# Performance work log

Measured on AMD Instinct MI355X. Metric: run time of the kernel, lower is better.

## Reference

```python
import jax, jax.numpy as jnp
import numpy as np

BS, T, N, M, P = 1024, 128, 128, 256, 256


def _lstm_cell(xin, h, c, Wih, Whh, bih, bhh):
    # PyTorch LSTMCell: gates ordered i, f, g, o
    z = xin @ Wih.T + bih + h @ Whh.T + bhh
    i, f, g, o = jnp.split(z, 4, axis=1)
    i = jax.nn.sigmoid(i); f = jax.nn.sigmoid(f)
    g = jnp.tanh(g); o = jax.nn.sigmoid(o)
    c2 = f * c + i * g
    return o * jnp.tanh(c2), c2


def setup_inputs() -> dict:
    key = jax.random.key(0)
    ks = jax.random.split(key, 24)
    s = 0.05
    return {
        "x": jax.random.normal(ks[0], (BS, T, N), jnp.float32),
        "y_known": jax.random.normal(ks[1], (BS, T, 1), jnp.float32),
        "We": jax.random.normal(ks[2], (T, 2 * M), jnp.float32) * s,
        "Ue": jax.random.normal(ks[3], (T, T), jnp.float32) * s,
        "Ve": jax.random.normal(ks[4], (1, T), jnp.float32) * s,
        "Wih_e": jax.random.normal(ks[5], (4 * M, N), jnp.float32) * s,
        "Whh_e": jax.random.normal(ks[6], (4 * M, M), jnp.float32) * s,
        "bih_e": jax.random.normal(ks[7], (4 * M,), jnp.float32) * s,
        "bhh_e": jax.random.normal(ks[8], (4 * M,), jnp.float32) * s,
        "Wd": jax.random.normal(ks[9], (M, 2 * P), jnp.float32) * s,
        "Ud": jax.random.normal(ks[10], (M, M), jnp.float32) * s,
        "Vd": jax.random.normal(ks[11], (1, M), jnp.float32) * s,
        "Wih_d": jax.random.normal(ks[12], (4 * P, 1), jnp.float32) * s,
        "Whh_d": jax.random.normal(ks[13], (4 * P, P), jnp.float32) * s,
        "bih_d": jax.random.normal(ks[14], (4 * P,), jnp.float32) * s,
        "bhh_d": jax.random.normal(ks[15], (4 * P,), jnp.float32) * s,
        "Wt": jax.random.normal(ks[16], (1, M + 1), jnp.float32) * s,
        "bt": jax.random.normal(ks[17], (1,), jnp.float32) * s,
        "W1": jax.random.normal(ks[18], (P, P + M), jnp.float32) * s,
        "b1": jax.random.normal(ks[19], (P,), jnp.float32) * s,
        "W2": jax.random.normal(ks[20], (1, P), jnp.float32) * s,
        "b2": jax.random.normal(ks[21], (1,), jnp.float32) * s,
    }


def reference(x, y_known, We, Ue, Ve, Wih_e, Whh_e, bih_e, bhh_e,
              Wd, Ud, Vd, Wih_d, Whh_d, bih_d, bhh_d,
              Wt, bt, W1, b1, W2, b2):
    bs, Tl, n = x.shape
    m = Whh_e.shape[1]
    p = Whh_d.shape[1]

    # ---- encoder (input attention) ----
    # U_e(x.permute(0,2,1)): loop-invariant, hoisted. (bs, n, T)
    Ux = jnp.einsum('btn,st->bns', x, Ue)

    def enc_step(carry, _):
        h, s = carry
        hs = jnp.concatenate([h, s], axis=1)            # (bs, 2m)
        ohs = hs @ We.T                                  # (bs, T)
        tanh_sum = jnp.tanh(ohs[:, None, :] + Ux)        # (bs, n, T)
        e = jnp.einsum('bnt,t->bn', tanh_sum, Ve[0])     # (bs, n)
        alpha = jax.nn.softmax(e, axis=1)
        xt = alpha * e                                   # faithful quirk: alpha * e_t
        h2, s2 = _lstm_cell(xt, h, s, Wih_e, Whh_e, bih_e, bhh_e)
        return (h2, s2), h2

    z = jnp.zeros((bs, m), x.dtype)
    _, h_all = jax.lax.scan(enc_step, (z, z), None, length=Tl)
    x1 = jnp.transpose(h_all, (1, 2, 0))                 # (bs, m, T)

    # ---- decoder (temporal attention) ----
    Udx = jnp.einsum('bmt,km->btk', x1, Ud)              # (bs, T, m)

    def dec_step(carry, yt):
        d, s, _ = carry
        ds = jnp.concatenate([d, s], axis=1)             # (bs, 2p)
        ods = ds @ Wd.T                                   # (bs, m)
        tanh_sum = jnp.tanh(ods[:, None, :] + Udx)        # (bs, T, m)
        l = jnp.einsum('btm,m->bt', tanh_sum, Vd[0])      # (bs, T)
        beta = jax.nn.softmax(l, axis=1)
        c = jnp.einsum('bt,bmt->bm', beta, x1)            # (bs, m)
        y_tilde = jnp.concatenate([yt, c], axis=1) @ Wt.T + bt  # (bs, 1)
        d2, s2 = _lstm_cell(y_tilde, d, s, Wih_d, Whh_d, bih_d, bhh_d)
        return (d2, s2, c), None

    zp = jnp.zeros((bs, p), x.dtype)
    zc = jnp.zeros((bs, m), x.dtype)
    (d, _, c), _ = jax.lax.scan(dec_step, (zp, zp, zc),
                                jnp.transpose(y_known, (1, 0, 2)))
    out1 = jnp.concatenate([d, c], axis=1) @ W1.T + b1
    return out1 @ W2.T + b2
```

## Files before the change

kernel.cpp:

```cpp
#include <hip/hip_runtime.h>


typedef unsigned int   uint;
typedef unsigned short ushort;
typedef _Float16 h2v __attribute__((ext_vector_type(2)));

#define O_WEH     0u
#define O_WENCH   32768u
#define O_WDH     229376u
#define O_WHHDH   294912u
#define O_UDT     425984u
#define O_UET     491520u
#define O_W1T     507904u
#define O_BENC    638976u
#define O_BDEC    640000u
#define W_FLOATS  641024u
#define O_X1H     641024u
#define O_BUF     17418240u
#define WS_FLOATS 34195456u

#define C2E 2.8853900817779268f
#define L2E 1.4426950408889634f

#define FMA4(acc, s, w) \
  acc.x = fmaf((s), (w).x, acc.x); \
  acc.y = fmaf((s), (w).y, acc.y); \
  acc.z = fmaf((s), (w).z, acc.z); \
  acc.w = fmaf((s), (w).w, acc.w);

union H2U { uint u; h2v h; _Float16 hs[2]; };

__device__ __forceinline__ float fdot2u(uint w, uint s, float acc) {
  H2U a; a.u = w; H2U b; b.u = s;
  return __builtin_amdgcn_fdot2(a.h, b.h, acc, false);
}
__device__ __forceinline__ uint pk2(float lo, float hi) {
  H2U v; v.hs[0] = (_Float16)lo; v.hs[1] = (_Float16)hi; return v.u;
}
__device__ __forceinline__ float h2lo(uint u) { H2U v; v.u = u; return (float)v.hs[0]; }
__device__ __forceinline__ float h2hi(uint u) { H2U v; v.u = u; return (float)v.hs[1]; }

__device__ __forceinline__ float fsig(float x) {
  return __builtin_amdgcn_rcpf(1.f + __builtin_amdgcn_exp2f(-L2E * x));
}
__device__ __forceinline__ float fth(float x) {
  float r = __builtin_amdgcn_rcpf(1.f + __builtin_amdgcn_exp2f(C2E * x));
  return fmaf(-2.f, r, 1.f);
}

#define DOT8(w, s0, s1) { \
  a0 = fdot2u(w.x, s0, a0); a1 = fdot2u(w.y, s0, a1); \
  a2 = fdot2u(w.z, s0, a2); a3 = fdot2u(w.w, s0, a3); \
  b0 = fdot2u(w.x, s1, b0); b1 = fdot2u(w.y, s1, b1); \
  b2 = fdot2u(w.z, s1, b2); b3 = fdot2u(w.w, s1, b3); }

#define ATT_TERM(vv, uu, oo) \
  ((vv) * __builtin_amdgcn_rcpf(1.f + __builtin_amdgcn_exp2f(fmaf(C2E, (uu), (oo)))))

__global__ __launch_bounds__(256) void prep_k(
    const float* __restrict__ We,    const float* __restrict__ Wih_e,
    const float* __restrict__ Whh_e, const float* __restrict__ Wd,
    const float* __restrict__ Whh_d, const float* __restrict__ W1,
    const float* __restrict__ Ud,    const float* __restrict__ Ue,
    const float* __restrict__ bih_e, const float* __restrict__ bhh_e,
    const float* __restrict__ bih_d, const float* __restrict__ bhh_d,
    float* __restrict__ ws)
{
  uint* wsu = (uint*)ws;
  unsigned idx = blockIdx.x * 256u + threadIdx.x;
  if (idx >= W_FLOATS) return;
  if (idx < 32768u) {
    unsigned kp = idx >> 7, j = idx & 127u;
    wsu[O_WEH + idx] = pk2(We[j * 512u + 2u*kp], We[j * 512u + 2u*kp + 1u]);
  } else if (idx < 229376u) {
    unsigned rel = idx - 32768u;
    unsigned kp = rel >> 10, j = rel & 1023u;
    float v0, v1;
    if (kp < 64u) { v0 = Wih_e[j * 128u + 2u*kp];          v1 = Wih_e[j * 128u + 2u*kp + 1u]; }
    else { unsigned k0 = 2u*(kp - 64u); v0 = Whh_e[j * 256u + k0]; v1 = Whh_e[j * 256u + k0 + 1u]; }
    wsu[O_WENCH + rel] = pk2(v0, v1);
  } else if (idx < 294912u) {
    unsigned rel = idx - 229376u;
    unsigned kp = rel >> 8, kk = rel & 255u;
    wsu[O_WDH + rel] = pk2(Wd[kk * 512u + 2u*kp], Wd[kk * 512u + 2u*kp + 1u]);
  } else if (idx < 425984u) {
    unsigned rel = idx - 294912u;
    unsigned kp = rel >> 10, j = rel & 1023u;
    wsu[O_WHHDH + rel] = pk2(Whh_d[j * 256u + 2u*kp], Whh_d[j * 256u + 2u*kp + 1u]);
  } else if (idx < 491520u) {
    unsigned rel = idx - 425984u;
    unsigned m = rel >> 8, k = rel & 255u;
    ws[O_UDT + rel] = Ud[k * 256u + m];
  } else if (idx < 507904u) {
    unsigned rel = idx - 491520u;
    unsigned t = rel >> 7, s = rel & 127u;
    ws[O_UET + rel] = Ue[s * 128u + t];
  } else if (idx < 638976u) {
    unsigned rel = idx - 507904u;
    unsigned k = rel >> 8, q = rel & 255u;
    ws[O_W1T + rel] = W1[q * 512u + k];
  } else if (idx < 640000u) {
    unsigned rel = idx - 638976u;
    ws[O_BENC + rel] = bih_e[rel] + bhh_e[rel];
  } else {
    unsigned rel = idx - 640000u;
    ws[O_BDEC + rel] = bih_d[rel] + bhh_d[rel];
  }
}

__global__ __launch_bounds__(256) void ux_k(
    const float* __restrict__ x, const float* __restrict__ UeT,
    uint* __restrict__ UxU)
{
  __shared__ float xs[128][32];
  const int b  = blockIdx.x >> 2;
  const int i0 = (blockIdx.x & 3) * 32;
  const int tid = threadIdx.x;
  for (int idx = tid; idx < 4096; idx += 256) {
    int t = idx >> 5, il = idx & 31;
    xs[t][il] = x[(size_t)b * 16384 + t * 128 + i0 + il];
  }
  __syncthreads();
  const int sl = tid & 31;
  const int ig = tid >> 5;
  const float4* UeT4 = (const float4*)UeT;
  float4 acc[4];
  #pragma unroll
  for (int ii = 0; ii < 4; ++ii) acc[ii] = make_float4(0.f, 0.f, 0.f, 0.f);
  for (int t = 0; t < 128; ++t) {
    float4 w = UeT4[t * 32 + sl];
    #pragma unroll
    for (int ii = 0; ii < 4; ++ii) {
      float a = xs[t][ig + 8 * ii];
      FMA4(acc[ii], a, w);
    }
  }
  uint2* U2 = (uint2*)UxU;
  #pragma unroll
  for (int ii = 0; ii < 4; ++ii) {
    int i_loc = i0 + ig + 8 * ii;
    uint2 pk;
    pk.x = pk2(acc[ii].x, acc[ii].y);
    pk.y = pk2(acc[ii].z, acc[ii].w);
    U2[((size_t)b * 128 + i_loc) * 32 + sl] = pk;
  }
}

__global__ __launch_bounds__(256) void udx_k(
    const uint* __restrict__ x1hU, const float* __restrict__ UdT,
    uint* __restrict__ UdxU)
{
  __shared__ float xs[32][256];
  const int b  = blockIdx.x >> 2;
  const int t0 = (blockIdx.x & 3) * 32;
  const int tid = threadIdx.x;
  const uint4* x14 = (const uint4*)x1hU + (size_t)b * 4096;
  for (int it = 0; it < 4; ++it) {
    int f = tid + it * 256;
    int tl = f >> 5, mq = f & 31;
    uint4 u = x14[(size_t)(t0 + tl) * 32 + mq];
    float* d = &xs[tl][mq * 8];
    d[0] = h2lo(u.x); d[1] = h2hi(u.x); d[2] = h2lo(u.y); d[3] = h2hi(u.y);
    d[4] = h2lo(u.z); d[5] = h2hi(u.z); d[6] = h2lo(u.w); d[7] = h2hi(u.w);
  }
  __syncthreads();
  const int kl = tid & 63;
  const int tg = tid >> 6;
  const float4* UdT4 = (const float4*)UdT;
  float4 acc[8];
  #pragma unroll
  for (int tt = 0; tt < 8; ++tt) acc[tt] = make_float4(0.f, 0.f, 0.f, 0.f);
  for (int m = 0; m < 256; ++m) {
    float4 w = UdT4[m * 64 + kl];
    #pragma unroll
    for (int tt = 0; tt < 8; ++tt) {
      float a = xs[tg + 4 * tt][m];
      FMA4(acc[tt], a, w);
    }
  }
  uint2* U2 = (uint2*)UdxU;
  #pragma unroll
  for (int tt = 0; tt < 8; ++tt) {
    uint2 pk;
    pk.x = pk2(acc[tt].x, acc[tt].y);
    pk.y = pk2(acc[tt].z, acc[tt].w);
    U2[((size_t)b * 128 + t0 + tg + 4 * tt) * 64 + kl] = pk;
  }
}

__global__ __launch_bounds__(512, 4) void encoder_k(
    const uint* __restrict__ WeH, const uint* __restrict__ WencH,
    const float* __restrict__ benc, const float* __restrict__ Ve,
    const uint* __restrict__ UxH, uint* __restrict__ x1hU)
{
  __shared__ uint stH[2][256];
  __shared__ uint xtH[2][64];
  __shared__ __align__(16) float part[4096];
  __shared__ float ohs2[2][128];
  __shared__ float bencS[1024];
  __shared__ float VeS[128];
  __shared__ float red[8];

  const int tid = threadIdx.x;
  const int b0 = blockIdx.x * 2;

  ((uint*)stH)[tid] = 0u;
  for (int i = tid; i < 1024; i += 512) bencS[i] = benc[i];
  if (tid < 128) VeS[tid] = Ve[tid];
  __syncthreads();

  float SVe = 0.f;
  for (int s = 0; s < 128; ++s) SVe += Ve[s];

  const uint4* WeH4   = (const uint4*)WeH;
  const uint4* WencH4 = (const uint4*)WencH;
  float4* part4 = (float4*)part;

  const int rB = tid >> 8, iB = (tid >> 1) & 127, sh = tid & 1;
  const uint4* ux4 = (const uint4*)UxH + ((size_t)(b0 + rB) * 128 + iB) * 16 + sh * 8;

  float c_reg = 0.f;

  for (int step = 0; step < 128; ++step) {
    {
      const int j4 = tid & 31, ks = tid >> 5;
      float a0=0,a1=0,a2=0,a3=0,b0=0,b1=0,b2=0,b3=0;
      const int kb = ks * 16;
      #pragma unroll 4
      for (int kp = kb; kp < kb + 16; ++kp) {
        uint4 w = WeH4[kp * 32 + j4];
        uint s0 = stH[0][kp], s1 = stH[1][kp];
        DOT8(w, s0, s1);
      }
      part4[(ks * 2 + 0) * 32 + j4] = make_float4(a0, a1, a2, a3);
      part4[(ks * 2 + 1) * 32 + j4] = make_float4(b0, b1, b2, b3);
    }
    __syncthreads();
    if (tid < 256) {
      const int r = tid >> 7, j = tid & 127;
      float acc = 0.f;
      #pragma unroll
      for (int ks = 0; ks < 16; ++ks) acc += part[(ks * 2 + r) * 128 + j];
      ohs2[r][j] = acc * C2E;
    }
    __syncthreads();
    float e_val;
    {
      float a0 = 0.f, a1 = 0.f, a2 = 0.f, a3 = 0.f;
      const float* oh = ohs2[rB];
      #pragma unroll 2
      for (int so = 0; so < 8; ++so) {
        uint4 u = ux4[so];
        const int s = sh * 64 + so * 8;
        a0 += ATT_TERM(VeS[s+0], h2lo(u.x), oh[s+0]);
        a1 += ATT_TERM(VeS[s+1], h2hi(u.x), oh[s+1]);
        a2 += ATT_TERM(VeS[s+2], h2lo(u.y), oh[s+2]);
        a3 += ATT_TERM(VeS[s+3], h2hi(u.y), oh[s+3]);
        a0 += ATT_TERM(VeS[s+4], h2lo(u.z), oh[s+4]);
        a1 += ATT_TERM(VeS[s+5], h2hi(u.z), oh[s+5]);
        a2 += ATT_TERM(VeS[s+6], h2lo(u.w), oh[s+6]);
        a3 += ATT_TERM(VeS[s+7], h2hi(u.w), oh[s+7]);
      }
      float r4 = (a0 + a1) + (a2 + a3);
      r4 += __shfl_xor(r4, 1);
      e_val = fmaf(-2.f, r4, SVe);
    }
    {
      float p  = __builtin_amdgcn_exp2f(L2E * e_val);
      float ps = (sh == 0) ? p : 0.f;
      #pragma unroll
      for (int o = 1; o < 64; o <<= 1) ps += __shfl_xor(ps, o);
      if ((tid & 63) == 0) red[tid >> 6] = ps;
      __syncthreads();
      const int base = (tid >> 6) & 4;
      float sm = (red[base+0] + red[base+1]) + (red[base+2] + red[base+3]);
      float xt = p * __builtin_amdgcn_rcpf(sm) * e_val;
      float xn = __shfl_down(xt, 2);
      if ((tid & 3) == 0) xtH[rB][iB >> 1] = pk2(xt, xn);
    }
    __syncthreads();
    {
      const int j4 = tid & 255, ks = tid >> 8;
      float a0=0,a1=0,a2=0,a3=0,b0=0,b1=0,b2=0,b3=0;
      if (ks == 0) {
        #pragma unroll 2
        for (int kp = 0; kp < 64; ++kp) {
          uint4 w = WencH4[kp * 256 + j4];
          uint s0 = xtH[0][kp], s1 = xtH[1][kp];
          DOT8(w, s0, s1);
        }
        #pragma unroll 2
        for (int kp = 64; kp < 96; ++kp) {
          uint4 w = WencH4[kp * 256 + j4];
          uint s0 = stH[0][kp - 64], s1 = stH[1][kp - 64];
          DOT8(w, s0, s1);
        }
      } else {
        #pragma unroll 2
        for (int kp = 96; kp < 192; ++kp) {
          uint4 w = WencH4[kp * 256 + j4];
          uint s0 = stH[0][kp - 64], s1 = stH[1][kp - 64];
          DOT8(w, s0, s1);
        }
      }
      part4[(ks * 2 + 0) * 256 + j4] = make_float4(a0, a1, a2, a3);
      part4[(ks * 2 + 1) * 256 + j4] = make_float4(b0, b1, b2, b3);
    }
    __syncthreads();
    {
      const int r = tid >> 8, j = tid & 255;
      float z0 = bencS[j]       + part[r * 1024 + j]       + part[(2 + r) * 1024 + j];
      float z1 = bencS[256 + j] + part[r * 1024 + 256 + j] + part[(2 + r) * 1024 + 256 + j];
      float z2 = bencS[512 + j] + part[r * 1024 + 512 + j] + part[(2 + r) * 1024 + 512 + j];
      float z3 = bencS[768 + j] + part[r * 1024 + 768 + j] + part[(2 + r) * 1024 + 768 + j];
      float gi = fsig(z0), gf = fsig(z1), gg = fth(z2), go = fsig(z3);
      float c2 = fmaf(gf, c_reg, gi * gg);
      c_reg = c2;
      float h2 = go * fth(c2);
      float hn = __shfl_down(h2, 1);
      float cn = __shfl_down(c2, 1);
      if (!(j & 1)) {
        uint hp = pk2(h2, hn), cp = pk2(c2, cn);
        stH[r][j >> 1] = hp;
        stH[r][128 + (j >> 1)] = cp;
        x1hU[((size_t)(b0 + r) * 128 + step) * 128 + (j >> 1)] = hp;
      }
    }
    __syncthreads();
  }
}

__global__ __launch_bounds__(512, 4) void decoder_k(
    const uint* __restrict__ WdH, const uint* __restrict__ WhhdH,
    const float* __restrict__ W1T, const float* __restrict__ bdec,
    const float* __restrict__ Vd,  const float* __restrict__ WihD,
    const float* __restrict__ Wt,  const float* __restrict__ btp,
    const float* __restrict__ b1,  const float* __restrict__ W2,
    const float* __restrict__ b2p, const float* __restrict__ yk,
    const uint* __restrict__ UdxH, const uint* __restrict__ x1hU,
    float* __restrict__ out)
{
  __shared__ uint stH[2][256];
  __shared__ __align__(16) float part[4096];
  __shared__ float ods2[2][256];
  __shared__ float cT[2][256];
  __shared__ float betaS[2][128];
  __shared__ float wihdS[1024];
  __shared__ float bdecS[1024];
  __shared__ float VdS[256];
  __shared__ float yts[2];
  __shared__ float red[8];

  const int tid = threadIdx.x;
  const int b0 = blockIdx.x * 2;

  ((uint*)stH)[tid] = 0u;
  for (int i = tid; i < 1024; i += 512) { wihdS[i] = WihD[i]; bdecS[i] = bdec[i]; }
  if (tid < 256) VdS[tid] = Vd[tid];
  __syncthreads();

  float SVd = 0.f;
  for (int k = 0; k < 256; ++k) SVd += Vd[k];

  const float bt0 = btp[0], Wt0 = Wt[0];
  const uint4*  WdH4   = (const uint4*)WdH;
  const uint4*  WhhdH4 = (const uint4*)WhhdH;
  const float4* W1T4   = (const float4*)W1T;
  float4* part4 = (float4*)part;

  const int rB = tid >> 8, tB = (tid >> 1) & 127, kh = tid & 1;
  const uint4* ud4 = (const uint4*)UdxH + ((size_t)(b0 + rB) * 128 + tB) * 32 + kh * 16;
  const int m8 = tid & 31, rb2 = (tid >> 5) & 1, ts = tid >> 6;
  const uint2* x12 = (const uint2*)x1hU + (size_t)(b0 + rb2) * 8192;

  float c_reg = 0.f;

  for (int step = 0; step < 128; ++step) {
    {
      const int j4 = tid & 63, ks = tid >> 6;
      float a0=0,a1=0,a2=0,a3=0,b0=0,b1=0,b2=0,b3=0;
      const int kb = ks * 32;
      #pragma unroll 4
      for (int kp = kb; kp < kb + 32; ++kp) {
        uint4 w = WdH4[kp * 64 + j4];
        uint s0 = stH[0][kp], s1 = stH[1][kp];
        DOT8(w, s0, s1);
      }
      part4[(ks * 2 + 0) * 64 + j4] = make_float4(a0, a1, a2, a3);
      part4[(ks * 2 + 1) * 64 + j4] = make_float4(b0, b1, b2, b3);
    }
    __syncthreads();
    {
      const int r = tid >> 8, kk = tid & 255;
      float acc = 0.f;
      #pragma unroll
      for (int ks = 0; ks < 8; ++ks) acc += part[(ks * 2 + r) * 256 + kk];
      ods2[r][kk] = acc * C2E;
    }
    __syncthreads();
    float l_val;
    {
      float a0 = 0.f, a1 = 0.f, a2 = 0.f, a3 = 0.f;
      const float* od = ods2[rB];
      #pragma unroll 2
      for (int ko = 0; ko < 16; ++ko) {
        uint4 u = ud4[ko];
        const int k = kh * 128 + ko * 8;
        a0 += ATT_TERM(VdS[k+0], h2lo(u.x), od[k+0]);
        a1 += ATT_TERM(VdS[k+1], h2hi(u.x), od[k+1]);
        a2 += ATT_TERM(VdS[k+2], h2lo(u.y), od[k+2]);
        a3 += ATT_TERM(VdS[k+3], h2hi(u.y), od[k+3]);
        a0 += ATT_TERM(VdS[k+4], h2lo(u.z), od[k+4]);
        a1 += ATT_TERM(VdS[k+5], h2hi(u.z), od[k+5]);
        a2 += ATT_TERM(VdS[k+6], h2lo(u.w), od[k+6]);
        a3 += ATT_TERM(VdS[k+7], h2hi(u.w), od[k+7]);
      }
      float r4 = (a0 + a1) + (a2 + a3);
      r4 += __shfl_xor(r4, 1);
      l_val = fmaf(-2.f, r4, SVd);
    }
    {
      float p  = __builtin_amdgcn_exp2f(L2E * l_val);
      float ps = (kh == 0) ? p : 0.f;
      #pragma unroll
      for (int o = 1; o < 64; o <<= 1) ps += __shfl_xor(ps, o);
      if ((tid & 63) == 0) red[tid >> 6] = ps;
      __syncthreads();
      const int base = (tid >> 6) & 4;
      float sm = (red[base+0] + red[base+1]) + (red[base+2] + red[base+3]);
      if (kh == 0) betaS[rB][tB] = p * __builtin_amdgcn_rcpf(sm);
    }
    __syncthreads();
    {
      float c0=0,c1=0,c2=0,c3=0,c4=0,c5=0,c6=0,c7=0;
      const float* bS = betaS[rb2];
      const uint2* xr = x12 + m8;
      #pragma unroll 4
      for (int tt = 0; tt < 16; ++tt) {
        const int t = ts * 16 + tt;
        float bv = bS[t];
        uint2 u  = xr[t * 64];
        uint2 u2 = xr[t * 64 + 32];
        c0 = fmaf(bv, h2lo(u.x),  c0); c1 = fmaf(bv, h2hi(u.x),  c1);
        c2 = fmaf(bv, h2lo(u.y),  c2); c3 = fmaf(bv, h2hi(u.y),  c3);
        c4 = fmaf(bv, h2lo(u2.x), c4); c5 = fmaf(bv, h2hi(u2.x), c5);
        c6 = fmaf(bv, h2lo(u2.y), c6); c7 = fmaf(bv, h2hi(u2.y), c7);
      }
      part4[(ts * 2 + rb2) * 64 + m8]      = make_float4(c0, c1, c2, c3);
      part4[(ts * 2 + rb2) * 64 + 32 + m8] = make_float4(c4, c5, c6, c7);
    }
    __syncthreads();
    {
      const int r = tid >> 8, m = tid & 255;
      float v = 0.f;
      #pragma unroll
      for (int t8 = 0; t8 < 8; ++t8) v += part[(t8 * 2 + r) * 256 + m];
      cT[r][m] = v;
      float pv = v * Wt[1 + m];
      #pragma unroll
      for (int o = 1; o < 64; o <<= 1) pv += __shfl_xor(pv, o);
      if ((tid & 63) == 0) red[tid >> 6] = pv;
      __syncthreads();
      if ((tid & 255) == 0) {
        const int base = r * 4;
        float s = (red[base] + red[base+1]) + (red[base+2] + red[base+3]);
        yts[r] = s + yk[(size_t)(b0 + r) * 128 + step] * Wt0 + bt0;
      }
    }
    {
      const int j4 = tid & 255, ks = tid >> 8;
      float a0=0,a1=0,a2=0,a3=0,b0=0,b1=0,b2=0,b3=0;
      const int kb = ks * 64;
      #pragma unroll 2
      for (int kp = kb; kp < kb + 64; ++kp) {
        uint4 w = WhhdH4[kp * 256 + j4];
        uint s0 = stH[0][kp], s1 = stH[1][kp];
        DOT8(w, s0, s1);
      }
      part4[(ks * 2 + 0) * 256 + j4] = make_float4(a0, a1, a2, a3);
      part4[(ks * 2 + 1) * 256 + j4] = make_float4(b0, b1, b2, b3);
    }
    __syncthreads();
    {
      const int r = tid >> 8, j = tid & 255;
      float yt = yts[r];
      float z0 = fmaf(yt, wihdS[j],       bdecS[j])       + part[r * 1024 + j]       + part[(2 + r) * 1024 + j];
      float z1 = fmaf(yt, wihdS[256 + j], bdecS[256 + j]) + part[r * 1024 + 256 + j] + part[(2 + r) * 1024 + 256 + j];
      float z2 = fmaf(yt, wihdS[512 + j], bdecS[512 + j]) + part[r * 1024 + 512 + j] + part[(2 + r) * 1024 + 512 + j];
      float z3 = fmaf(yt, wihdS[768 + j], bdecS[768 + j]) + part[r * 1024 + 768 + j] + part[(2 + r) * 1024 + 768 + j];
      float gi = fsig(z0), gf = fsig(z1), gg = fth(z2), go = fsig(z3);
      float c2 = fmaf(gf, c_reg, gi * gg);
      c_reg = c2;
      float d2 = go * fth(c2);
      float dn = __shfl_down(d2, 1);
      float cn = __shfl_down(c2, 1);
      if (!(j & 1)) {
        stH[r][j >> 1] = pk2(d2, dn);
        stH[r][128 + (j >> 1)] = pk2(c2, cn);
      }
    }
    __syncthreads();
  }
  {
    const int l = tid & 63, ks = tid >> 6;
    float a0=0,a1=0,a2=0,a3=0,b0=0,b1=0,b2=0,b3=0;
    const int kb = ks * 64;
    if (ks < 4) {
      for (int k = kb; k < kb + 64; ++k) {
        float4 w = W1T4[k * 64 + l];
        uint u0 = stH[0][k >> 1], u1 = stH[1][k >> 1];
        float d0 = (k & 1) ? h2hi(u0) : h2lo(u0);
        float d1 = (k & 1) ? h2hi(u1) : h2lo(u1);
        a0=fmaf(d0,w.x,a0); a1=fmaf(d0,w.y,a1); a2=fmaf(d0,w.z,a2); a3=fmaf(d0,w.w,a3);
        b0=fmaf(d1,w.x,b0); b1=fmaf(d1,w.y,b1); b2=fmaf(d1,w.z,b2); b3=fmaf(d1,w.w,b3);
      }
    } else {
      for (int k = kb; k < kb + 64; ++k) {
        float4 w = W1T4[k * 64 + l];
        float c0 = cT[0][k - 256], c1 = cT[1][k - 256];
        a0=fmaf(c0,w.x,a0); a1=fmaf(c0,w.y,a1); a2=fmaf(c0,w.z,a2); a3=fmaf(c0,w.w,a3);
        b0=fmaf(c1,w.x,b0); b1=fmaf(c1,w.y,b1); b2=fmaf(c1,w.z,b2); b3=fmaf(c1,w.w,b3);
      }
    }
    part4[(ks * 2 + 0) * 64 + l] = make_float4(a0, a1, a2, a3);
    part4[(ks * 2 + 1) * 64 + l] = make_float4(b0, b1, b2, b3);
  }
  __syncthreads();
  {
    const int r = tid >> 8, q = tid & 255;
    float o1 = b1[q];
    #pragma unroll
    for (int ks = 0; ks < 8; ++ks) o1 += part[(ks * 2 + r) * 256 + q];
    float pv = o1 * W2[q];
    #pragma unroll
    for (int o = 1; o < 64; o <<= 1) pv += __shfl_xor(pv, o);
    if ((tid & 63) == 0) red[tid >> 6] = pv;
    __syncthreads();
    if ((tid & 255) == 0) {
      const int base = r * 4;
      float s = (red[base] + red[base+1]) + (red[base+2] + red[base+3]);
      out[b0 + r] = s + b2p[0];
    }
  }
}

extern "C" void kernel_launch(void* const* d_in, const int* in_sizes, int n_in,
                              void* d_out, int out_size, void* d_ws, size_t ws_size,
                              hipStream_t stream)
{
  const float* x       = (const float*)d_in[0];
  const float* y_known = (const float*)d_in[1];
  const float* We      = (const float*)d_in[2];
  const float* Ue      = (const float*)d_in[3];
  const float* Ve      = (const float*)d_in[4];
  const float* Wih_e   = (const float*)d_in[5];
  const float* Whh_e   = (const float*)d_in[6];
  const float* bih_e   = (const float*)d_in[7];
  const float* bhh_e   = (const float*)d_in[8];
  const float* Wd      = (const float*)d_in[9];
  const float* Ud      = (const float*)d_in[10];
  const float* Vd      = (const float*)d_in[11];
  const float* Wih_d   = (const float*)d_in[12];
  const float* Whh_d   = (const float*)d_in[13];
  const float* bih_d   = (const float*)d_in[14];
  const float* bhh_d   = (const float*)d_in[15];
  const float* Wt      = (const float*)d_in[16];
  const float* bt      = (const float*)d_in[17];
  const float* W1      = (const float*)d_in[18];
  const float* b1      = (const float*)d_in[19];
  const float* W2      = (const float*)d_in[20];
  const float* b2      = (const float*)d_in[21];

  float* ws  = (float*)d_ws;
  float* out = (float*)d_out;
  if (ws_size < (size_t)WS_FLOATS * 4u) return;

  uint* wsu  = (uint*)ws;
  uint* x1hU = (uint*)(ws + O_X1H);
  uint* bufU = (uint*)(ws + O_BUF);

  prep_k<<<(W_FLOATS + 255) / 256, 256, 0, stream>>>(
      We, Wih_e, Whh_e, Wd, Whh_d, W1, Ud, Ue,
      bih_e, bhh_e, bih_d, bhh_d, ws);

  ux_k<<<4096, 256, 0, stream>>>(x, ws + O_UET, bufU);
  encoder_k<<<512, 512, 0, stream>>>(wsu + O_WEH, wsu + O_WENCH,
                                     ws + O_BENC, Ve, bufU, x1hU);
  udx_k<<<4096, 256, 0, stream>>>(x1hU, ws + O_UDT, bufU);
  decoder_k<<<512, 512, 0, stream>>>(wsu + O_WDH, wsu + O_WHHDH,
                                     ws + O_W1T, ws + O_BDEC, Vd, Wih_d,
                                     Wt, bt, b1, W2, b2, y_known,
                                     bufU, x1hU, out);
}
```

Measured before the change: 7.277 ms.

## Process one batch row per block in encoder and decoder kernels

Restructures the encoder and decoder recurrent kernels so each 256-thread block handles a single batch row instead of two rows per 512-thread block, doubling the grid size. This shortens per-step reductions and the shared-memory footprint, and simplifies the final MLP to a direct per-thread dot product. In exchange, each weight load from global/L2 is reused for only one row, doubling weight traffic per step.

```diff
diff --git a/kernel.cpp b/kernel.cpp
--- a/kernel.cpp
+++ b/kernel.cpp
@@ -48,11 +48,9 @@
   return fmaf(-2.f, r, 1.f);
 }
 
-#define DOT8(w, s0, s1) { \
+#define DOT4(w, s0) { \
   a0 = fdot2u(w.x, s0, a0); a1 = fdot2u(w.y, s0, a1); \
-  a2 = fdot2u(w.z, s0, a2); a3 = fdot2u(w.w, s0, a3); \
-  b0 = fdot2u(w.x, s1, b0); b1 = fdot2u(w.y, s1, b1); \
-  b2 = fdot2u(w.z, s1, b2); b3 = fdot2u(w.w, s1, b3); }
+  a2 = fdot2u(w.z, s0, a2); a3 = fdot2u(w.w, s0, a3); }
 
 #define ATT_TERM(vv, uu, oo) \
   ((vv) * __builtin_amdgcn_rcpf(1.f + __builtin_amdgcn_exp2f(fmaf(C2E, (uu), (oo)))))
@@ -188,24 +186,25 @@
   }
 }
 
-__global__ __launch_bounds__(512, 4) void encoder_k(
+__global__ __launch_bounds__(256, 4) void encoder_k(
     const uint* __restrict__ WeH, const uint* __restrict__ WencH,
     const float* __restrict__ benc, const float* __restrict__ Ve,
     const uint* __restrict__ UxH, uint* __restrict__ x1hU)
 {
-  __shared__ uint stH[2][256];
-  __shared__ uint xtH[2][64];
-  __shared__ __align__(16) float part[4096];
-  __shared__ float ohs2[2][128];
+  __shared__ uint stH[256];
+  __shared__ uint xtH[64];
+  __shared__ __align__(16) float part[1024];
+  __shared__ float ohs2[128];
   __shared__ float bencS[1024];
   __shared__ float VeS[128];
-  __shared__ float red[8];
+  __shared__ float red1[4];
 
   const int tid = threadIdx.x;
-  const int b0 = blockIdx.x * 2;
-
-  ((uint*)stH)[tid] = 0u;
-  for (int i = tid; i < 1024; i += 512) bencS[i] = benc[i];
+  const int b = blockIdx.x;
+
+  stH[tid] = 0u;
+  #pragma unroll
+  for (int i = 0; i < 4; ++i) bencS[tid + i * 256] = benc[tid + i * 256];
   if (tid < 128) VeS[tid] = Ve[tid];
   __syncthreads();
 
@@ -216,50 +215,47 @@
   const uint4* WencH4 = (const uint4*)WencH;
   float4* part4 = (float4*)part;
 
-  const int rB = tid >> 8, iB = (tid >> 1) & 127, sh = tid & 1;
-  const uint4* ux4 = (const uint4*)UxH + ((size_t)(b0 + rB) * 128 + iB) * 16 + sh * 8;
+  const int iB = tid >> 1, sh = tid & 1;
+  const uint4* ux4 = (const uint4*)UxH + ((size_t)b * 128 + iB) * 16 + sh * 8;
 
   float c_reg = 0.f;
 
   for (int step = 0; step < 128; ++step) {
     {
       const int j4 = tid & 31, ks = tid >> 5;
-      float a0=0,a1=0,a2=0,a3=0,b0=0,b1=0,b2=0,b3=0;
-      const int kb = ks * 16;
+      float a0 = 0.f, a1 = 0.f, a2 = 0.f, a3 = 0.f;
+      const int kb = ks * 32;
       #pragma unroll 4
-      for (int kp = kb; kp < kb + 16; ++kp) {
+      for (int kp = kb; kp < kb + 32; ++kp) {
         uint4 w = WeH4[kp * 32 + j4];
-        uint s0 = stH[0][kp], s1 = stH[1][kp];
-        DOT8(w, s0, s1);
-      }
-      part4[(ks * 2 + 0) * 32 + j4] = make_float4(a0, a1, a2, a3);
-      part4[(ks * 2 + 1) * 32 + j4] = make_float4(b0, b1, b2, b3);
-    }
-    __syncthreads();
-    if (tid < 256) {
-      const int r = tid >> 7, j = tid & 127;
+        uint s0 = stH[kp];
+        DOT4(w, s0);
+      }
+      part4[ks * 32 + j4] = make_float4(a0, a1, a2, a3);
+    }
+    __syncthreads();
+    if (tid < 128) {
       float acc = 0.f;
       #pragma unroll
-      for (int ks = 0; ks < 16; ++ks) acc += part[(ks * 2 + r) * 128 + j];
-      ohs2[r][j] = acc * C2E;
+      for (int ks = 0; ks < 8; ++ks) acc += part[ks * 128 + tid];
+      ohs2[tid] = acc * C2E;
     }
     __syncthreads();
     float e_val;
     {
       float a0 = 0.f, a1 = 0.f, a2 = 0.f, a3 = 0.f;
-      const float* oh = ohs2[rB];
       #pragma unroll 2
       for (int so = 0; so < 8; ++so) {
         uint4 u = ux4[so];
         const int s = sh * 64 + so * 8;
-        a0 += ATT_TERM(VeS[s+0], h2lo(u.x), oh[s+0]);
-        a1 += ATT_TERM(VeS[s+1], h2hi(u.x), oh[s+1]);
-        a2 += ATT_TERM(VeS[s+2], h2lo(u.y), oh[s+2]);
-        a3 += ATT_TERM(VeS[s+3], h2hi(u.y), oh[s+3]);
-        a0 += ATT_TERM(VeS[s+4], h2lo(u.z), oh[s+4]);
-        a1 += ATT_TERM(VeS[s+5], h2hi(u.z), oh[s+5]);
-        a2 += ATT_TERM(VeS[s+6], h2lo(u.w), oh[s+6]);
-        a3 += ATT_TERM(VeS[s+7], h2hi(u.w), oh[s+7]);
+        a0 += ATT_TERM(VeS[s+0], h2lo(u.x), ohs2[s+0]);
+        a1 += ATT_TERM(VeS[s+1], h2hi(u.x), ohs2[s+1]);
+        a2 += ATT_TERM(VeS[s+2], h2lo(u.y), ohs2[s+2]);
+        a3 += ATT_TERM(VeS[s+3], h2hi(u.y), ohs2[s+3]);
+        a0 += ATT_TERM(VeS[s+4], h2lo(u.z), ohs2[s+4]);
+        a1 += ATT_TERM(VeS[s+5], h2hi(u.z), ohs2[s+5]);
+        a2 += ATT_TERM(VeS[s+6], h2lo(u.w), ohs2[s+6]);
+        a3 += ATT_TERM(VeS[s+7], h2hi(u.w), ohs2[s+7]);
       }
       float r4 = (a0 + a1) + (a2 + a3);
       r4 += __shfl_xor(r4, 1);
@@ -270,49 +266,37 @@
       float ps = (sh == 0) ? p : 0.f;
       #pragma unroll
       for (int o = 1; o < 64; o <<= 1) ps += __shfl_xor(ps, o);
-      if ((tid & 63) == 0) red[tid >> 6] = ps;
+      if ((tid & 63) == 0) red1[tid >> 6] = ps;
       __syncthreads();
-      const int base = (tid >> 6) & 4;
-      float sm = (red[base+0] + red[base+1]) + (red[base+2] + red[base+3]);
+      float sm = (red1[0] + red1[1]) + (red1[2] + red1[3]);
       float xt = p * __builtin_amdgcn_rcpf(sm) * e_val;
       float xn = __shfl_down(xt, 2);
-      if ((tid & 3) == 0) xtH[rB][iB >> 1] = pk2(xt, xn);
-    }
-    __syncthreads();
-    {
-      const int j4 = tid & 255, ks = tid >> 8;
-      float a0=0,a1=0,a2=0,a3=0,b0=0,b1=0,b2=0,b3=0;
-      if (ks == 0) {
-        #pragma unroll 2
-        for (int kp = 0; kp < 64; ++kp) {
-          uint4 w = WencH4[kp * 256 + j4];
-          uint s0 = xtH[0][kp], s1 = xtH[1][kp];
-          DOT8(w, s0, s1);
-        }
-        #pragma unroll 2
-        for (int kp = 64; kp < 96; ++kp) {
-          uint4 w = WencH4[kp * 256 + j4];
-          uint s0 = stH[0][kp - 64], s1 = stH[1][kp - 64];
-          DOT8(w, s0, s1);
-        }
-      } else {
-        #pragma unroll 2
-        for (int kp = 96; kp < 192; ++kp) {
-          uint4 w = WencH4[kp * 256 + j4];
-          uint s0 = stH[0][kp - 64], s1 = stH[1][kp - 64];
-          DOT8(w, s0, s1);
-        }
-      }
-      part4[(ks * 2 + 0) * 256 + j4] = make_float4(a0, a1, a2, a3);
-      part4[(ks * 2 + 1) * 256 + j4] = make_float4(b0, b1, b2, b3);
-    }
-    __syncthreads();
-    {
-      const int r = tid >> 8, j = tid & 255;
-      float z0 = bencS[j]       + part[r * 1024 + j]       + part[(2 + r) * 1024 + j];
-      float z1 = bencS[256 + j] + part[r * 1024 + 256 + j] + part[(2 + r) * 1024 + 256 + j];
-      float z2 = bencS[512 + j] + part[r * 1024 + 512 + j] + part[(2 + r) * 1024 + 512 + j];
-      float z3 = bencS[768 + j] + part[r * 1024 + 768 + j] + part[(2 + r) * 1024 + 768 + j];
+      if ((tid & 3) == 0) xtH[iB >> 1] = pk2(xt, xn);
+    }
+    __syncthreads();
+    {
+      float a0 = 0.f, a1 = 0.f, a2 = 0.f, a3 = 0.f;
+      #pragma unroll 2
+      for (int kp = 0; kp < 64; ++kp) {
+        uint4 w = WencH4[kp * 256 + tid];
+        uint s0 = xtH[kp];
+        DOT4(w, s0);
+      }
+      #pragma unroll 2
+      for (int kp = 64; kp < 192; ++kp) {
+        uint4 w = WencH4[kp * 256 + tid];
+        uint s0 = stH[kp - 64];
+        DOT4(w, s0);
+      }
+      part4[tid] = make_float4(a0, a1, a2, a3);
+    }
+    __syncthreads();
+    {
+      const int j = tid;
+      float z0 = bencS[j]       + part[j];
+      float z1 = bencS[256 + j] + part[256 + j];
+      float z2 = bencS[512 + j] + part[512 + j];
+      float z3 = bencS[768 + j] + part[768 + j];
       float gi = fsig(z0), gf = fsig(z1), gg = fth(z2), go = fsig(z3);
       float c2 = fmaf(gf, c_reg, gi * gg);
       c_reg = c2;
@@ -321,16 +305,16 @@
       float cn = __shfl_down(c2, 1);
       if (!(j & 1)) {
         uint hp = pk2(h2, hn), cp = pk2(c2, cn);
-        stH[r][j >> 1] = hp;
-        stH[r][128 + (j >> 1)] = cp;
-        x1hU[((size_t)(b0 + r) * 128 + step) * 128 + (j >> 1)] = hp;
-      }
-    }
-    __syncthreads();
-  }
-}
-
-__global__ __launch_bounds__(512, 4) void decoder_k(
+        stH[j >> 1] = hp;
+        stH[128 + (j >> 1)] = cp;
+        x1hU[((size_t)b * 128 + step) * 128 + (j >> 1)] = hp;
+      }
+    }
+    __syncthreads();
+  }
+}
+
+__global__ __launch_bounds__(256, 4) void decoder_k(
     const uint* __restrict__ WdH, const uint* __restrict__ WhhdH,
     const float* __restrict__ W1T, const float* __restrict__ bdec,
     const float* __restrict__ Vd,  const float* __restrict__ WihD,
@@ -340,23 +324,29 @@
     const uint* __restrict__ UdxH, const uint* __restrict__ x1hU,
     float* __restrict__ out)
 {
-  __shared__ uint stH[2][256];
-  __shared__ __align__(16) float part[4096];
-  __shared__ float ods2[2][256];
-  __shared__ float cT[2][256];
-  __shared__ float betaS[2][128];
+  __shared__ uint stH[256];
+  __shared__ __align__(16) float part[2048];
+  __shared__ float ods2[256];
+  __shared__ float cT[256];
+  __shared__ float betaS[128];
   __shared__ float wihdS[1024];
   __shared__ float bdecS[1024];
   __shared__ float VdS[256];
-  __shared__ float yts[2];
-  __shared__ float red[8];
+  __shared__ float ytS;
+  __shared__ float red1[4];
+  __shared__ float red2[4];
+  __shared__ float red3[4];
 
   const int tid = threadIdx.x;
-  const int b0 = blockIdx.x * 2;
-
-  ((uint*)stH)[tid] = 0u;
-  for (int i = tid; i < 1024; i += 512) { wihdS[i] = WihD[i]; bdecS[i] = bdec[i]; }
-  if (tid < 256) VdS[tid] = Vd[tid];
+  const int b = blockIdx.x;
+
+  stH[tid] = 0u;
+  #pragma unroll
+  for (int i = 0; i < 4; ++i) {
+    wihdS[tid + i * 256] = WihD[tid + i * 256];
+    bdecS[tid + i * 256] = bdec[tid + i * 256];
+  }
+  VdS[tid] = Vd[tid];
   __syncthreads();
 
   float SVd = 0.f;
@@ -365,55 +355,50 @@
   const float bt0 = btp[0], Wt0 = Wt[0];
   const uint4*  WdH4   = (const uint4*)WdH;
   const uint4*  WhhdH4 = (const uint4*)WhhdH;
-  const float4* W1T4   = (const float4*)W1T;
+  const float*  W1Tf   = W1T;
   float4* part4 = (float4*)part;
 
-  const int rB = tid >> 8, tB = (tid >> 1) & 127, kh = tid & 1;
-  const uint4* ud4 = (const uint4*)UdxH + ((size_t)(b0 + rB) * 128 + tB) * 32 + kh * 16;
-  const int m8 = tid & 31, rb2 = (tid >> 5) & 1, ts = tid >> 6;
-  const uint2* x12 = (const uint2*)x1hU + (size_t)(b0 + rb2) * 8192;
+  const int tB = tid >> 1, kh = tid & 1;
+  const uint4* ud4 = (const uint4*)UdxH + ((size_t)b * 128 + tB) * 32 + kh * 16;
+  const int mc = tid & 31, ts = tid >> 5;
+  const uint2* x12 = (const uint2*)x1hU + (size_t)b * 8192;
 
   float c_reg = 0.f;
 
   for (int step = 0; step < 128; ++step) {
     {
       const int j4 = tid & 63, ks = tid >> 6;
-      float a0=0,a1=0,a2=0,a3=0,b0=0,b1=0,b2=0,b3=0;
-      const int kb = ks * 32;
+      float a0 = 0.f, a1 = 0.f, a2 = 0.f, a3 = 0.f;
+      const int kb = ks * 64;
       #pragma unroll 4
-      for (int kp = kb; kp < kb + 32; ++kp) {
+      for (int kp = kb; kp < kb + 64; ++kp) {
         uint4 w = WdH4[kp * 64 + j4];
-        uint s0 = stH[0][kp], s1 = stH[1][kp];
-        DOT8(w, s0, s1);
-      }
-      part4[(ks * 2 + 0) * 64 + j4] = make_float4(a0, a1, a2, a3);
-      part4[(ks * 2 + 1) * 64 + j4] = make_float4(b0, b1, b2, b3);
-    }
-    __syncthreads();
-    {
-      const int r = tid >> 8, kk = tid & 255;
-      float acc = 0.f;
-      #pragma unroll
-      for (int ks = 0; ks < 8; ++ks) acc += part[(ks * 2 + r) * 256 + kk];
-      ods2[r][kk] = acc * C2E;
+        uint s0 = stH[kp];
+        DOT4(w, s0);
+      }
+      part4[ks * 64 + j4] = make_float4(a0, a1, a2, a3);
+    }
+    __syncthreads();
+    {
+      float acc = part[tid] + part[256 + tid] + part[512 + tid] + part[768 + tid];
+      ods2[tid] = acc * C2E;
     }
     __syncthreads();
     float l_val;
     {
       float a0 = 0.f, a1 = 0.f, a2 = 0.f, a3 = 0.f;
-      const float* od = ods2[rB];
       #pragma unroll 2
       for (int ko = 0; ko < 16; ++ko) {
         uint4 u = ud4[ko];
         const int k = kh * 128 + ko * 8;
-        a0 += ATT_TERM(VdS[k+0], h2lo(u.x), od[k+0]);
-        a1 += ATT_TERM(VdS[k+1], h2hi(u.x), od[k+1]);
-        a2 += ATT_TERM(VdS[k+2], h2lo(u.y), od[k+2]);
-        a3 += ATT_TERM(VdS[k+3], h2hi(u.y), od[k+3]);
-        a0 += ATT_TERM(VdS[k+4], h2lo(u.z), od[k+4]);
-        a1 += ATT_TERM(VdS[k+5], h2hi(u.z), od[k+5]);
-        a2 += ATT_TERM(VdS[k+6], h2lo(u.w), od[k+6]);
-        a3 += ATT_TERM(VdS[k+7], h2hi(u.w), od[k+7]);
+        a0 += ATT_TERM(VdS[k+0], h2lo(u.x), ods2[k+0]);
+        a1 += ATT_TERM(VdS[k+1], h2hi(u.x), ods2[k+1]);
+        a2 += ATT_TERM(VdS[k+2], h2lo(u.y), ods2[k+2]);
+        a3 += ATT_TERM(VdS[k+3], h2hi(u.y), ods2[k+3]);
+        a0 += ATT_TERM(VdS[k+4], h2lo(u.z), ods2[k+4]);
+        a1 += ATT_TERM(VdS[k+5], h2hi(u.z), ods2[k+5]);
+        a2 += ATT_TERM(VdS[k+6], h2lo(u.w), ods2[k+6]);
+        a3 += ATT_TERM(VdS[k+7], h2hi(u.w), ods2[k+7]);
       }
       float r4 = (a0 + a1) + (a2 + a3);
       r4 += __shfl_xor(r4, 1);
@@ -424,21 +409,19 @@
       float ps = (kh == 0) ? p : 0.f;
       #pragma unroll
       for (int o = 1; o < 64; o <<= 1) ps += __shfl_xor(ps, o);
-      if ((tid & 63) == 0) red[tid >> 6] = ps;
+      if ((tid & 63) == 0) red1[tid >> 6] = ps;
       __syncthreads();
-      const int base = (tid >> 6) & 4;
-      float sm = (red[base+0] + red[base+1]) + (red[base+2] + red[base+3]);
-      if (kh == 0) betaS[rB][tB] = p * __builtin_amdgcn_rcpf(sm);
+      float sm = (red1[0] + red1[1]) + (red1[2] + red1[3]);
+      if (kh == 0) betaS[tB] = p * __builtin_amdgcn_rcpf(sm);
     }
     __syncthreads();
     {
       float c0=0,c1=0,c2=0,c3=0,c4=0,c5=0,c6=0,c7=0;
-      const float* bS = betaS[rb2];
-      const uint2* xr = x12 + m8;
+      const uint2* xr = x12 + mc;
       #pragma unroll 4
       for (int tt = 0; tt < 16; ++tt) {
         const int t = ts * 16 + tt;
-        float bv = bS[t];
+        float bv = betaS[t];
         uint2 u  = xr[t * 64];
         uint2 u2 = xr[t * 64 + 32];
         c0 = fmaf(bv, h2lo(u.x),  c0); c1 = fmaf(bv, h2hi(u.x),  c1);
@@ -446,48 +429,44 @@
         c4 = fmaf(bv, h2lo(u2.x), c4); c5 = fmaf(bv, h2hi(u2.x), c5);
         c6 = fmaf(bv, h2lo(u2.y), c6); c7 = fmaf(bv, h2hi(u2.y), c7);
       }
-      part4[(ts * 2 + rb2) * 64 + m8]      = make_float4(c0, c1, c2, c3);
-      part4[(ts * 2 + rb2) * 64 + 32 + m8] = make_float4(c4, c5, c6, c7);
-    }
-    __syncthreads();
-    {
-      const int r = tid >> 8, m = tid & 255;
+      part4[ts * 64 + mc]      = make_float4(c0, c1, c2, c3);
+      part4[ts * 64 + 32 + mc] = make_float4(c4, c5, c6, c7);
+    }
+    __syncthreads();
+    {
       float v = 0.f;
       #pragma unroll
-      for (int t8 = 0; t8 < 8; ++t8) v += part[(t8 * 2 + r) * 256 + m];
-      cT[r][m] = v;
-      float pv = v * Wt[1 + m];
+      for (int t8 = 0; t8 < 8; ++t8) v += part[t8 * 256 + tid];
+      cT[tid] = v;
+      float pv = v * Wt[1 + tid];
       #pragma unroll
       for (int o = 1; o < 64; o <<= 1) pv += __shfl_xor(pv, o);
-      if ((tid & 63) == 0) red[tid >> 6] = pv;
+      if ((tid & 63) == 0) red2[tid >> 6] = pv;
       __syncthreads();
-      if ((tid & 255) == 0) {
-        const int base = r * 4;
-        float s = (red[base] + red[base+1]) + (red[base+2] + red[base+3]);
-        yts[r] = s + yk[(size_t)(b0 + r) * 128 + step] * Wt0 + bt0;
-      }
-    }
-    {
-      const int j4 = tid & 255, ks = tid >> 8;
-      float a0=0,a1=0,a2=0,a3=0,b0=0,b1=0,b2=0,b3=0;
-      const int kb = ks * 64;
+      if (tid == 0) {
+        float s = (red2[0] + red2[1]) + (red2[2] + red2[3]);
+        ytS = s + yk[(size_t)b * 128 + step] * Wt0 + bt0;
+      }
+    }
+    __syncthreads();
+    {
+      float a0 = 0.f, a1 = 0.f, a2 = 0.f, a3 = 0.f;
       #pragma unroll 2
-      for (int kp = kb; kp < kb + 64; ++kp) {
-        uint4 w = WhhdH4[kp * 256 + j4];
-        uint s0 = stH[0][kp], s1 = stH[1][kp];
-        DOT8(w, s0, s1);
-      }
-      part4[(ks * 2 + 0) * 256 + j4] = make_float4(a0, a1, a2, a3);
-      part4[(ks * 2 + 1) * 256 + j4] = make_float4(b0, b1, b2, b3);
-    }
-    __syncthreads();
-    {
-      const int r = tid >> 8, j = tid & 255;
-      float yt = yts[r];
-      float z0 = fmaf(yt, wihdS[j],       bdecS[j])       + part[r * 1024 + j]       + part[(2 + r) * 1024 + j];
-      float z1 = fmaf(yt, wihdS[256 + j], bdecS[256 + j]) + part[r * 1024 + 256 + j] + part[(2 + r) * 1024 + 256 + j];
-      float z2 = fmaf(yt, wihdS[512 + j], bdecS[512 + j]) + part[r * 1024 + 512 + j] + part[(2 + r) * 1024 + 512 + j];
-      float z3 = fmaf(yt, wihdS[768 + j], bdecS[768 + j]) + part[r * 1024 + 768 + j] + part[(2 + r) * 1024 + 768 + j];
+      for (int kp = 0; kp < 128; ++kp) {
+        uint4 w = WhhdH4[kp * 256 + tid];
+        uint s0 = stH[kp];
+        DOT4(w, s0);
+      }
+      part4[tid] = make_float4(a0, a1, a2, a3);
+    }
+    __syncthreads();
+    {
+      const int j = tid;
+      float yt = ytS;
+      float z0 = fmaf(yt, wihdS[j],       bdecS[j])       + part[j];
+      float z1 = fmaf(yt, wihdS[256 + j], bdecS[256 + j]) + part[256 + j];
+      float z2 = fmaf(yt, wihdS[512 + j], bdecS[512 + j]) + part[512 + j];
+      float z3 = fmaf(yt, wihdS[768 + j], bdecS[768 + j]) + part[768 + j];
       float gi = fsig(z0), gf = fsig(z1), gg = fth(z2), go = fsig(z3);
       float c2 = fmaf(gf, c_reg, gi * gg);
       c_reg = c2;
@@ -495,51 +474,32 @@
       float dn = __shfl_down(d2, 1);
       float cn = __shfl_down(c2, 1);
       if (!(j & 1)) {
-        stH[r][j >> 1] = pk2(d2, dn);
-        stH[r][128 + (j >> 1)] = pk2(c2, cn);
+        stH[j >> 1] = pk2(d2, dn);
+        stH[128 + (j >> 1)] = pk2(c2, cn);
       }
     }
     __syncthreads();
   }
   {
-    const int l = tid & 63, ks = tid >> 6;
-    float a0=0,a1=0,a2=0,a3=0,b0=0,b1=0,b2=0,b3=0;
-    const int kb = ks * 64;
-    if (ks < 4) {
-      for (int k = kb; k < kb + 64; ++k) {
-        float4 w = W1T4[k * 64 + l];
-        uint u0 = stH[0][k >> 1], u1 = stH[1][k >> 1];
-        float d0 = (k & 1) ? h2hi(u0) : h2lo(u0);
-        float d1 = (k & 1) ? h2hi(u1) : h2lo(u1);
-        a0=fmaf(d0,w.x,a0); a1=fmaf(d0,w.y,a1); a2=fmaf(d0,w.z,a2); a3=fmaf(d0,w.w,a3);
-        b0=fmaf(d1,w.x,b0); b1=fmaf(d1,w.y,b1); b2=fmaf(d1,w.z,b2); b3=fmaf(d1,w.w,b3);
-      }
-    } else {
-      for (int k = kb; k < kb + 64; ++k) {
-        float4 w = W1T4[k * 64 + l];
-        float c0 = cT[0][k - 256], c1 = cT[1][k - 256];
-        a0=fmaf(c0,w.x,a0); a1=fmaf(c0,w.y,a1); a2=fmaf(c0,w.z,a2); a3=fmaf(c0,w.w,a3);
-        b0=fmaf(c1,w.x,b0); b1=fmaf(c1,w.y,b1); b2=fmaf(c1,w.z,b2); b3=fmaf(c1,w.w,b3);
-      }
-    }
-    part4[(ks * 2 + 0) * 64 + l] = make_float4(a0, a1, a2, a3);
-    part4[(ks * 2 + 1) * 64 + l] = make_float4(b0, b1, b2, b3);
-  }
-  __syncthreads();
-  {
-    const int r = tid >> 8, q = tid & 255;
+    const int q = tid;
     float o1 = b1[q];
-    #pragma unroll
-    for (int ks = 0; ks < 8; ++ks) o1 += part[(ks * 2 + r) * 256 + q];
+    #pragma unroll 4
+    for (int k = 0; k < 256; ++k) {
+      uint u0 = stH[k >> 1];
+      float dv = (k & 1) ? h2hi(u0) : h2lo(u0);
+      o1 = fmaf(dv, W1Tf[k * 256 + q], o1);
+    }
+    #pragma unroll 4
+    for (int k = 256; k < 512; ++k) {
+      o1 = fmaf(cT[k - 256], W1Tf[k * 256 + q], o1);
+    }
     float pv = o1 * W2[q];
     #pragma unroll
     for (int o = 1; o < 64; o <<= 1) pv += __shfl_xor(pv, o);
-    if ((tid & 63) == 0) red[tid >> 6] = pv;
-    __syncthreads();
-    if ((tid & 255) == 0) {
-      const int base = r * 4;
-      float s = (red[base] + red[base+1]) + (red[base+2] + red[base+3]);
-      out[b0 + r] = s + b2p[0];
+    if ((tid & 63) == 0) red3[tid >> 6] = pv;
+    __syncthreads();
+    if (tid == 0) {
+      out[b] = (red3[0] + red3[1]) + (red3[2] + red3[3]) + b2p[0];
     }
   }
 }
@@ -584,11 +544,11 @@
       bih_e, bhh_e, bih_d, bhh_d, ws);
 
   ux_k<<<4096, 256, 0, stream>>>(x, ws + O_UET, bufU);
-  encoder_k<<<512, 512, 0, stream>>>(wsu + O_WEH, wsu + O_WENCH,
-                                     ws + O_BENC, Ve, bufU, x1hU);
+  encoder_k<<<1024, 256, 0, stream>>>(wsu + O_WEH, wsu + O_WENCH,
+                                      ws + O_BENC, Ve, bufU, x1hU);
   udx_k<<<4096, 256, 0, stream>>>(x1hU, ws + O_UDT, bufU);
-  decoder_k<<<512, 512, 0, stream>>>(wsu + O_WDH, wsu + O_WHHDH,
-                                     ws + O_W1T, ws + O_BDEC, Vd, Wih_d,
-                                     Wt, bt, b1, W2, b2, y_known,
-                                     bufU, x1hU, out);
-}
+  decoder_k<<<1024, 256, 0, stream>>>(wsu + O_WDH, wsu + O_WHHDH,
+                                      ws + O_W1T, ws + O_BDEC, Vd, Wih_d,
+                                      Wt, bt, b1, W2, b2, y_known,
+                                      bufU, x1hU, out);
+}
```

Result: slower. 9.482 ms (+30.3%).
